# Kernel tuning notes

Measured on AMD Instinct MI355X. Metric: run time of the kernel, lower is better.

The kernel has to match this reference:

```python
import jax, jax.numpy as jnp
import numpy as np

N_NODES = 20000
N_EDGES = 640000
IN_DIM = 128
HID = 128
OUT_DIM = 3
N_GRAPHS = 32


def setup_inputs() -> dict:
    key = jax.random.key(0)
    ks = jax.random.split(key, 12)
    x = jax.random.normal(ks[0], (N_NODES, IN_DIM), dtype=jnp.float32)
    edge_index = jax.random.randint(ks[1], (2, N_EDGES), 0, N_NODES, dtype=jnp.int64)
    batch = jnp.sort(jax.random.randint(ks[2], (N_NODES,), 0, N_GRAPHS, dtype=jnp.int64))
    batch = batch.at[0].set(0).at[-1].set(N_GRAPHS - 1)
    s = 0.05
    W_gcn = jax.random.normal(ks[3], (IN_DIM, HID), jnp.float32) * s
    b_gcn = jnp.zeros((HID,), jnp.float32)
    W_sage_l = jax.random.normal(ks[4], (HID, HID), jnp.float32) * s  # neighbor branch
    W_sage_r = jax.random.normal(ks[5], (HID, HID), jnp.float32) * s  # root branch
    b_sage = jnp.zeros((HID,), jnp.float32)
    W_fc1 = jax.random.normal(ks[6], (HID, HID), jnp.float32) * s
    b_fc1 = jnp.zeros((HID,), jnp.float32)
    W_fc2 = jax.random.normal(ks[7], (HID, OUT_DIM), jnp.float32) * s
    b_fc2 = jnp.zeros((OUT_DIM,), jnp.float32)
    return {
        'x': x, 'edge_index': edge_index, 'batch': batch,
        'W_gcn': W_gcn, 'b_gcn': b_gcn,
        'W_sage_l': W_sage_l, 'W_sage_r': W_sage_r, 'b_sage': b_sage,
        'W_fc1': W_fc1, 'b_fc1': b_fc1, 'W_fc2': W_fc2, 'b_fc2': b_fc2,
    }


def reference(x, edge_index, batch, W_gcn, b_gcn, W_sage_l, W_sage_r, b_sage,
              W_fc1, b_fc1, W_fc2, b_fc2):
    n = x.shape[0]
    row, col = edge_index[0], edge_index[1]  # source -> target

    # ---- GCNConv: symmetric-normalized aggregation with self-loops ----
    h = x @ W_gcn  # [N, H]
    loops = jnp.arange(n, dtype=row.dtype)
    row_sl = jnp.concatenate([row, loops])
    col_sl = jnp.concatenate([col, loops])
    deg = jax.ops.segment_sum(jnp.ones_like(col_sl, dtype=h.dtype), col_sl,
                              num_segments=n)
    dinv = jnp.where(deg > 0, jax.lax.rsqrt(deg), 0.0)
    norm = dinv[row_sl] * dinv[col_sl]  # [E+N]
    h_gcn = jax.ops.segment_sum(h[row_sl] * norm[:, None], col_sl,
                                num_segments=n) + b_gcn
    h_gcn = jax.nn.relu(h_gcn)

    # ---- SAGEConv (mean aggregator) ----
    cnt = jax.ops.segment_sum(jnp.ones_like(col, dtype=h_gcn.dtype), col,
                              num_segments=n)
    neigh = jax.ops.segment_sum(h_gcn[row], col, num_segments=n)
    neigh = neigh / jnp.maximum(cnt, 1.0)[:, None]
    h_sage = neigh @ W_sage_l + h_gcn @ W_sage_r + b_sage
    h_sage = jax.nn.relu(h_sage)

    # ---- global_add_pool (num_graphs = 32 < 50) ----
    pooled = jax.ops.segment_sum(h_sage, batch, num_segments=N_GRAPHS)  # [G, H]

    # ---- MLP head ----
    out = jax.nn.relu(pooled @ W_fc1 + b_fc1) @ W_fc2 + b_fc2  # [G, 3]
    return out
```

## Files before the change

### kernel.cpp

```cpp
#include <hip/hip_runtime.h>

#define N_NODES 20000
#define N_EDGES 640000
#define HID 128
#define N_GRAPHS 32

#define SCAN_BLK 256
#define SCAN_NBLK ((N_NODES + SCAN_BLK - 1) / SCAN_BLK)

__global__ __launch_bounds__(256) void hist_k(const int* __restrict__ col,
                                              int* __restrict__ cnt) {
    int e = blockIdx.x * blockDim.x + threadIdx.x;
    if (e < N_EDGES) {
        int c = col[e];
        if ((unsigned)c < N_NODES) atomicAdd(&cnt[c], 1);
    }
}

__global__ __launch_bounds__(SCAN_BLK) void scanA_k(const int* __restrict__ cnt,
                                                    int* __restrict__ blkSum) {
    __shared__ int wsum[SCAN_BLK / 64];
    const int b = blockIdx.x, t = threadIdx.x;
    const int i = b * SCAN_BLK + t;
    int v = (i < N_NODES) ? cnt[i] : 0;
#pragma unroll
    for (int o = 1; o < 64; o <<= 1) v += __shfl_xor(v, o);
    if ((t & 63) == 0) wsum[t >> 6] = v;
    __syncthreads();
    if (t == 0) {
        int s = 0;
#pragma unroll
        for (int w = 0; w < SCAN_BLK / 64; ++w) s += wsum[w];
        blkSum[b] = s;
    }
}

__global__ __launch_bounds__(SCAN_BLK) void scanB_k(const int* __restrict__ cnt,
                                                    const int* __restrict__ blkSum,
                                                    int* __restrict__ offs,
                                                    int* __restrict__ cursor,
                                                    float* __restrict__ dinv) {
    __shared__ int sm[SCAN_BLK];
    __shared__ int base_s;
    const int b = blockIdx.x, t = threadIdx.x;
    const int i = b * SCAN_BLK + t;
    const int v = (i < N_NODES) ? cnt[i] : 0;
    sm[t] = v;
    if (t == 0) {
        int s = 0;
        for (int k = 0; k < b; ++k) s += blkSum[k];
        base_s = s;
    }
    __syncthreads();
    for (int o = 1; o < SCAN_BLK; o <<= 1) {
        int add = (t >= o) ? sm[t - o] : 0;
        __syncthreads();
        sm[t] += add;
        __syncthreads();
    }
    if (i < N_NODES) {
        int excl = base_s + ((t > 0) ? sm[t - 1] : 0);
        offs[i] = excl;
        cursor[i] = excl;
        dinv[i] = rsqrtf((float)(v + 1));
        if (i == N_NODES - 1) offs[N_NODES] = excl + v;
    }
}

__global__ __launch_bounds__(256) void fill_k(const int* __restrict__ row,
                                              const int* __restrict__ col,
                                              int* __restrict__ cursor,
                                              int* __restrict__ csr_src) {
    int e = blockIdx.x * blockDim.x + threadIdx.x;
    if (e < N_EDGES) {
        int c = col[e];
        int r = row[e];
        if ((unsigned)c < N_NODES && (unsigned)r < N_NODES) {
            int p = atomicAdd(&cursor[c], 1);
            csr_src[p] = r;
        }
    }
}

__global__ __launch_bounds__(256) void gemm128_k(const float* __restrict__ X,
                                                 const float* __restrict__ W,
                                                 float* __restrict__ Y) {
    __shared__ float wbuf[64 * 128];
    const int t = threadIdx.x;
    const int lane = t & 63;
    const int wid = __builtin_amdgcn_readfirstlane(t >> 6);
    const int c2 = lane * 2;
    const int row0 = blockIdx.x * 32 + wid * 8;
    const float* Xr = X + (size_t)row0 * 128;
    float2 acc[8];
#pragma unroll
    for (int r = 0; r < 8; ++r) acc[r] = make_float2(0.f, 0.f);
#pragma unroll
    for (int kc = 0; kc < 2; ++kc) {
        __syncthreads();
#pragma unroll
        for (int i = 0; i < 8; ++i)
            ((float4*)wbuf)[t + i * 256] = ((const float4*)W)[kc * 2048 + t + i * 256];
        __syncthreads();
        const int kb = kc * 64;
        for (int k0 = 0; k0 < 64; k0 += 4) {
            float4 xa[8];
#pragma unroll
            for (int r = 0; r < 8; ++r)
                xa[r] = *(const float4*)&Xr[r * 128 + kb + k0];
#pragma unroll
            for (int kk = 0; kk < 4; ++kk) {
                float2 w = *(const float2*)&wbuf[(k0 + kk) * 128 + c2];
#pragma unroll
                for (int r = 0; r < 8; ++r) {
                    float xv = (&xa[r].x)[kk];
                    acc[r].x = fmaf(xv, w.x, acc[r].x);
                    acc[r].y = fmaf(xv, w.y, acc[r].y);
                }
            }
        }
    }
#pragma unroll
    for (int r = 0; r < 8; ++r)
        *(float2*)&Y[(size_t)(row0 + r) * 128 + c2] = acc[r];
}

__global__ __launch_bounds__(256) void gcn_agg_k(const float* __restrict__ h,
                                                 const int* __restrict__ offs,
                                                 const int* __restrict__ src,
                                                 const float* __restrict__ dinv,
                                                 const float* __restrict__ bias,
                                                 float* __restrict__ out) {
    const int wave = threadIdx.x >> 6;
    const int lane = threadIdx.x & 63;
    const int half = lane >> 5;
    const int node = (blockIdx.x * 4 + wave) * 2 + half;
    const int c4 = (lane & 31) * 4;
    const int nd = (node < N_NODES) ? node : (N_NODES - 1);
    const float dc = dinv[nd];
    float4 hv = *(const float4*)&h[(size_t)nd * 128 + c4];
    float4 acc = make_float4(dc * hv.x, dc * hv.y, dc * hv.z, dc * hv.w);
    const int beg = offs[nd];
    const int deg = offs[nd + 1] - beg;
    const int mdeg = max(deg, __shfl(deg, lane ^ 32));
    for (int j = 0; j < mdeg; j += 4) {
        int i0 = (j + 0 < deg) ? beg + j + 0 : 0;
        int i1 = (j + 1 < deg) ? beg + j + 1 : 0;
        int i2 = (j + 2 < deg) ? beg + j + 2 : 0;
        int i3 = (j + 3 < deg) ? beg + j + 3 : 0;
        int s0 = src[i0], s1 = src[i1], s2 = src[i2], s3 = src[i3];
        float w0 = (j + 0 < deg) ? dinv[s0] : 0.f;
        float w1 = (j + 1 < deg) ? dinv[s1] : 0.f;
        float w2 = (j + 2 < deg) ? dinv[s2] : 0.f;
        float w3 = (j + 3 < deg) ? dinv[s3] : 0.f;
        float4 v0 = *(const float4*)&h[(size_t)s0 * 128 + c4];
        float4 v1 = *(const float4*)&h[(size_t)s1 * 128 + c4];
        float4 v2 = *(const float4*)&h[(size_t)s2 * 128 + c4];
        float4 v3 = *(const float4*)&h[(size_t)s3 * 128 + c4];
        acc.x = fmaf(w0, v0.x, fmaf(w1, v1.x, fmaf(w2, v2.x, fmaf(w3, v3.x, acc.x))));
        acc.y = fmaf(w0, v0.y, fmaf(w1, v1.y, fmaf(w2, v2.y, fmaf(w3, v3.y, acc.y))));
        acc.z = fmaf(w0, v0.z, fmaf(w1, v1.z, fmaf(w2, v2.z, fmaf(w3, v3.z, acc.z))));
        acc.w = fmaf(w0, v0.w, fmaf(w1, v1.w, fmaf(w2, v2.w, fmaf(w3, v3.w, acc.w))));
    }
    float4 b = *(const float4*)&bias[c4];
    float4 o;
    o.x = fmaxf(fmaf(dc, acc.x, b.x), 0.f);
    o.y = fmaxf(fmaf(dc, acc.y, b.y), 0.f);
    o.z = fmaxf(fmaf(dc, acc.z, b.z), 0.f);
    o.w = fmaxf(fmaf(dc, acc.w, b.w), 0.f);
    if (node < N_NODES) *(float4*)&out[(size_t)node * 128 + c4] = o;
}

__global__ __launch_bounds__(256) void sage_agg_k(const float* __restrict__ hg,
                                                  const int* __restrict__ offs,
                                                  const int* __restrict__ src,
                                                  float* __restrict__ out) {
    const int wave = threadIdx.x >> 6;
    const int lane = threadIdx.x & 63;
    const int half = lane >> 5;
    const int node = (blockIdx.x * 4 + wave) * 2 + half;
    const int c4 = (lane & 31) * 4;
    const int nd = (node < N_NODES) ? node : (N_NODES - 1);
    float4 acc = make_float4(0.f, 0.f, 0.f, 0.f);
    const int beg = offs[nd];
    const int deg = offs[nd + 1] - beg;
    const int mdeg = max(deg, __shfl(deg, lane ^ 32));
    for (int j = 0; j < mdeg; j += 4) {
        int i0 = (j + 0 < deg) ? beg + j + 0 : 0;
        int i1 = (j + 1 < deg) ? beg + j + 1 : 0;
        int i2 = (j + 2 < deg) ? beg + j + 2 : 0;
        int i3 = (j + 3 < deg) ? beg + j + 3 : 0;
        float w0 = (j + 0 < deg) ? 1.f : 0.f;
        float w1 = (j + 1 < deg) ? 1.f : 0.f;
        float w2 = (j + 2 < deg) ? 1.f : 0.f;
        float w3 = (j + 3 < deg) ? 1.f : 0.f;
        int s0 = src[i0], s1 = src[i1], s2 = src[i2], s3 = src[i3];
        float4 v0 = *(const float4*)&hg[(size_t)s0 * 128 + c4];
        float4 v1 = *(const float4*)&hg[(size_t)s1 * 128 + c4];
        float4 v2 = *(const float4*)&hg[(size_t)s2 * 128 + c4];
        float4 v3 = *(const float4*)&hg[(size_t)s3 * 128 + c4];
        acc.x = fmaf(w0, v0.x, fmaf(w1, v1.x, fmaf(w2, v2.x, fmaf(w3, v3.x, acc.x))));
        acc.y = fmaf(w0, v0.y, fmaf(w1, v1.y, fmaf(w2, v2.y, fmaf(w3, v3.y, acc.y))));
        acc.z = fmaf(w0, v0.z, fmaf(w1, v1.z, fmaf(w2, v2.z, fmaf(w3, v3.z, acc.z))));
        acc.w = fmaf(w0, v0.w, fmaf(w1, v1.w, fmaf(w2, v2.w, fmaf(w3, v3.w, acc.w))));
    }
    float inv = 1.0f / (float)max(deg, 1);
    float4 o;
    o.x = acc.x * inv;
    o.y = acc.y * inv;
    o.z = acc.z * inv;
    o.w = acc.w * inv;
    if (node < N_NODES) *(float4*)&out[(size_t)node * 128 + c4] = o;
}

__global__ __launch_bounds__(256) void combine_k(const float* __restrict__ An,
                                                 const float* __restrict__ Bh,
                                                 const float* __restrict__ Wl,
                                                 const float* __restrict__ Wr,
                                                 const float* __restrict__ bias,
                                                 float* __restrict__ Y) {
    __shared__ float wbuf[64 * 128];
    const int t = threadIdx.x;
    const int lane = t & 63;
    const int wid = __builtin_amdgcn_readfirstlane(t >> 6);
    const int c2 = lane * 2;
    const int row0 = blockIdx.x * 32 + wid * 8;
    float2 acc[8];
    {
        float2 b = *(const float2*)&bias[c2];
#pragma unroll
        for (int r = 0; r < 8; ++r) acc[r] = b;
    }
#pragma unroll
    for (int m = 0; m < 2; ++m) {
        const float* Wm = m ? Wr : Wl;
        const float* Xr = (m ? Bh : An) + (size_t)row0 * 128;
#pragma unroll
        for (int kc = 0; kc < 2; ++kc) {
            __syncthreads();
#pragma unroll
            for (int i = 0; i < 8; ++i)
                ((float4*)wbuf)[t + i * 256] = ((const float4*)Wm)[kc * 2048 + t + i * 256];
            __syncthreads();
            const int kb = kc * 64;
            for (int k0 = 0; k0 < 64; k0 += 4) {
                float4 xa[8];
#pragma unroll
                for (int r = 0; r < 8; ++r)
                    xa[r] = *(const float4*)&Xr[r * 128 + kb + k0];
#pragma unroll
                for (int kk = 0; kk < 4; ++kk) {
                    float2 w = *(const float2*)&wbuf[(k0 + kk) * 128 + c2];
#pragma unroll
                    for (int r = 0; r < 8; ++r) {
                        float xv = (&xa[r].x)[kk];
                        acc[r].x = fmaf(xv, w.x, acc[r].x);
                        acc[r].y = fmaf(xv, w.y, acc[r].y);
                    }
                }
            }
        }
    }
#pragma unroll
    for (int r = 0; r < 8; ++r) {
        float2 o = acc[r];
        o.x = fmaxf(o.x, 0.f);
        o.y = fmaxf(o.y, 0.f);
        *(float2*)&Y[(size_t)(row0 + r) * 128 + c2] = o;
    }
}

#define POOL_ROWS 64
__global__ __launch_bounds__(256) void pool_k(const float* __restrict__ H,
                                              const int* __restrict__ batch,
                                              float* __restrict__ pooled) {
    const int r0 = blockIdx.x * POOL_ROWS;
    const int t = threadIdx.x;
    const int d = t & 127, half = t >> 7;
    const int rend = min(r0 + POOL_ROWS, N_NODES);
    int i = r0 + half;
    if (i >= rend) return;
    int cur = batch[i];
    float acc = 0.f;
    for (; i < rend; i += 2) {
        int g = batch[i];
        if (g != cur) {
            atomicAdd(&pooled[cur * 128 + d], acc);
            acc = 0.f;
            cur = g;
        }
        acc += H[(size_t)i * 128 + d];
    }
    atomicAdd(&pooled[cur * 128 + d], acc);
}

__global__ __launch_bounds__(128) void head_k(const float* __restrict__ pooled,
                                              const float* __restrict__ Wfc1,
                                              const float* __restrict__ bfc1,
                                              const float* __restrict__ Wfc2,
                                              const float* __restrict__ bfc2,
                                              float* __restrict__ out) {
    __shared__ float pl[128];
    __shared__ float tmp[128];
    const int g = blockIdx.x;
    const int t = threadIdx.x;
    pl[t] = pooled[g * 128 + t];
    __syncthreads();
    float a = bfc1[t];
#pragma unroll 8
    for (int k = 0; k < 128; ++k) a = fmaf(pl[k], Wfc1[k * 128 + t], a);
    tmp[t] = fmaxf(a, 0.f);
    __syncthreads();
    if (t < 3) {
        float a2 = bfc2[t];
        for (int k = 0; k < 128; ++k) a2 = fmaf(tmp[k], Wfc2[k * 3 + t], a2);
        out[g * 3 + t] = a2;
    }
}

extern "C" void kernel_launch(void* const* d_in, const int* in_sizes, int n_in,
                              void* d_out, int out_size, void* d_ws, size_t ws_size,
                              hipStream_t stream) {
    const float* x      = (const float*)d_in[0];
    const int*   ei     = (const int*)d_in[1];
    const int*   batch  = (const int*)d_in[2];
    const float* W_gcn  = (const float*)d_in[3];
    const float* b_gcn  = (const float*)d_in[4];
    const float* W_sl   = (const float*)d_in[5];
    const float* W_sr   = (const float*)d_in[6];
    const float* b_sage = (const float*)d_in[7];
    const float* W_fc1  = (const float*)d_in[8];
    const float* b_fc1  = (const float*)d_in[9];
    const float* W_fc2  = (const float*)d_in[10];
    const float* b_fc2  = (const float*)d_in[11];
    float* out = (float*)d_out;

    char* base = (char*)d_ws;
    size_t off = 0;
    auto take = [&](size_t bytes) -> void* {
        void* p = base + off;
        off += (bytes + 255) & ~(size_t)255;
        return p;
    };
    int*   cnt      = (int*)take((size_t)N_NODES * 4);
    int*   offs     = (int*)take((size_t)(N_NODES + 1) * 4);
    int*   cursor   = (int*)take((size_t)N_NODES * 4);
    float* dinv     = (float*)take((size_t)N_NODES * 4);
    int*   blkSum   = (int*)take((size_t)SCAN_NBLK * 4);
    int*   csr_src  = (int*)take((size_t)N_EDGES * 4);
    float* bufA     = (float*)take((size_t)N_NODES * HID * 4);
    float* bufB     = (float*)take((size_t)N_NODES * HID * 4);
    float* pooled   = (float*)take((size_t)N_GRAPHS * HID * 4);

    const int* row = ei;
    const int* col = ei + N_EDGES;

    hipMemsetAsync(cnt, 0, (size_t)N_NODES * 4, stream);
    hipMemsetAsync(pooled, 0, (size_t)N_GRAPHS * HID * 4, stream);

    hist_k<<<(N_EDGES + 255) / 256, 256, 0, stream>>>(col, cnt);
    scanA_k<<<SCAN_NBLK, SCAN_BLK, 0, stream>>>(cnt, blkSum);
    scanB_k<<<SCAN_NBLK, SCAN_BLK, 0, stream>>>(cnt, blkSum, offs, cursor, dinv);
    fill_k<<<(N_EDGES + 255) / 256, 256, 0, stream>>>(row, col, cursor, csr_src);

    const int gemm_blocks = N_NODES / 32;
    const int agg_blocks = (N_NODES + 7) / 8;
    gemm128_k<<<gemm_blocks, 256, 0, stream>>>(x, W_gcn, bufA);
    gcn_agg_k<<<agg_blocks, 256, 0, stream>>>(bufA, offs, csr_src, dinv, b_gcn, bufB);
    sage_agg_k<<<agg_blocks, 256, 0, stream>>>(bufB, offs, csr_src, bufA);
    combine_k<<<gemm_blocks, 256, 0, stream>>>(bufA, bufB, W_sl, W_sr, b_sage, bufA);
    pool_k<<<(N_NODES + POOL_ROWS - 1) / POOL_ROWS, 256, 0, stream>>>(bufA, batch, pooled);
    head_k<<<N_GRAPHS, 128, 0, stream>>>(pooled, W_fc1, b_fc1, W_fc2, b_fc2, out);
}
```

Measured before the change: 330.0 us.

## Stage transposed X tile in LDS and use 4x4 register tiles in GEMMs

The two dense GEMM kernels (the GCN projection and the SAGE combine) now stage the block's 32 input rows into shared memory, transposed and padded. Each thread then computes a 4-row by 4-column tile using float4 loads from both X and W in LDS. Before, each thread did an 8x2 tile and read X straight from global memory. The aim is fewer global loads per FMA and better register reuse, at the cost of extra LDS space and transpose stores that may bank-conflict, which could lower occupancy.

```diff
diff --git a/kernel.cpp b/kernel.cpp
--- a/kernel.cpp
+++ b/kernel.cpp
@@ -7,6 +7,8 @@
 
 #define SCAN_BLK 256
 #define SCAN_NBLK ((N_NODES + SCAN_BLK - 1) / SCAN_BLK)
+
+#define XT_STRIDE 36
 
 __global__ __launch_bounds__(256) void hist_k(const int* __restrict__ col,
                                               int* __restrict__ cnt) {
@@ -82,47 +84,70 @@
     }
 }
 
+__device__ __forceinline__ void stage_xt(float* xt, const float* __restrict__ Xm,
+                                         int row0, int t) {
+    const int r = t & 31;
+    const int kbase = (t >> 5) * 16;
+    const float* xp = Xm + (size_t)(row0 + r) * 128 + kbase;
+#pragma unroll
+    for (int c = 0; c < 4; ++c) {
+        float4 v = *(const float4*)&xp[c * 4];
+        xt[(kbase + c * 4 + 0) * XT_STRIDE + r] = v.x;
+        xt[(kbase + c * 4 + 1) * XT_STRIDE + r] = v.y;
+        xt[(kbase + c * 4 + 2) * XT_STRIDE + r] = v.z;
+        xt[(kbase + c * 4 + 3) * XT_STRIDE + r] = v.w;
+    }
+}
+
+__device__ __forceinline__ void gemm_half(const float* xt, const float* wbuf,
+                                          int kb, int rg, int c4, float4 acc[4]) {
+#pragma unroll 8
+    for (int k0 = 0; k0 < 64; ++k0) {
+        float4 w = *(const float4*)&wbuf[k0 * 128 + c4];
+        float4 xr = *(const float4*)&xt[(kb + k0) * XT_STRIDE + rg * 4];
+        acc[0].x = fmaf(xr.x, w.x, acc[0].x);
+        acc[0].y = fmaf(xr.x, w.y, acc[0].y);
+        acc[0].z = fmaf(xr.x, w.z, acc[0].z);
+        acc[0].w = fmaf(xr.x, w.w, acc[0].w);
+        acc[1].x = fmaf(xr.y, w.x, acc[1].x);
+        acc[1].y = fmaf(xr.y, w.y, acc[1].y);
+        acc[1].z = fmaf(xr.y, w.z, acc[1].z);
+        acc[1].w = fmaf(xr.y, w.w, acc[1].w);
+        acc[2].x = fmaf(xr.z, w.x, acc[2].x);
+        acc[2].y = fmaf(xr.z, w.y, acc[2].y);
+        acc[2].z = fmaf(xr.z, w.z, acc[2].z);
+        acc[2].w = fmaf(xr.z, w.w, acc[2].w);
+        acc[3].x = fmaf(xr.w, w.x, acc[3].x);
+        acc[3].y = fmaf(xr.w, w.y, acc[3].y);
+        acc[3].z = fmaf(xr.w, w.z, acc[3].z);
+        acc[3].w = fmaf(xr.w, w.w, acc[3].w);
+    }
+}
+
 __global__ __launch_bounds__(256) void gemm128_k(const float* __restrict__ X,
                                                  const float* __restrict__ W,
                                                  float* __restrict__ Y) {
     __shared__ float wbuf[64 * 128];
+    __shared__ float xt[128 * XT_STRIDE];
     const int t = threadIdx.x;
-    const int lane = t & 63;
-    const int wid = __builtin_amdgcn_readfirstlane(t >> 6);
-    const int c2 = lane * 2;
-    const int row0 = blockIdx.x * 32 + wid * 8;
-    const float* Xr = X + (size_t)row0 * 128;
-    float2 acc[8];
-#pragma unroll
-    for (int r = 0; r < 8; ++r) acc[r] = make_float2(0.f, 0.f);
+    const int rg = t >> 5;
+    const int c4 = (t & 31) * 4;
+    const int row0 = blockIdx.x * 32;
+    float4 acc[4];
+    acc[0] = acc[1] = acc[2] = acc[3] = make_float4(0.f, 0.f, 0.f, 0.f);
+    stage_xt(xt, X, row0, t);
 #pragma unroll
     for (int kc = 0; kc < 2; ++kc) {
-        __syncthreads();
+        if (kc) __syncthreads();
 #pragma unroll
         for (int i = 0; i < 8; ++i)
             ((float4*)wbuf)[t + i * 256] = ((const float4*)W)[kc * 2048 + t + i * 256];
         __syncthreads();
-        const int kb = kc * 64;
-        for (int k0 = 0; k0 < 64; k0 += 4) {
-            float4 xa[8];
-#pragma unroll
-            for (int r = 0; r < 8; ++r)
-                xa[r] = *(const float4*)&Xr[r * 128 + kb + k0];
-#pragma unroll
-            for (int kk = 0; kk < 4; ++kk) {
-                float2 w = *(const float2*)&wbuf[(k0 + kk) * 128 + c2];
-#pragma unroll
-                for (int r = 0; r < 8; ++r) {
-                    float xv = (&xa[r].x)[kk];
-                    acc[r].x = fmaf(xv, w.x, acc[r].x);
-                    acc[r].y = fmaf(xv, w.y, acc[r].y);
-                }
-            }
-        }
-    }
-#pragma unroll
-    for (int r = 0; r < 8; ++r)
-        *(float2*)&Y[(size_t)(row0 + r) * 128 + c2] = acc[r];
+        gemm_half(xt, wbuf, kc * 64, rg, c4, acc);
+    }
+#pragma unroll
+    for (int i = 0; i < 4; ++i)
+        *(float4*)&Y[(size_t)(row0 + rg * 4 + i) * 128 + c4] = acc[i];
 }
 
 __global__ __launch_bounds__(256) void gcn_agg_k(const float* __restrict__ h,
@@ -220,53 +245,40 @@
                                                  const float* __restrict__ bias,
                                                  float* __restrict__ Y) {
     __shared__ float wbuf[64 * 128];
+    __shared__ float xt[128 * XT_STRIDE];
     const int t = threadIdx.x;
-    const int lane = t & 63;
-    const int wid = __builtin_amdgcn_readfirstlane(t >> 6);
-    const int c2 = lane * 2;
-    const int row0 = blockIdx.x * 32 + wid * 8;
-    float2 acc[8];
+    const int rg = t >> 5;
+    const int c4 = (t & 31) * 4;
+    const int row0 = blockIdx.x * 32;
+    float4 acc[4];
     {
-        float2 b = *(const float2*)&bias[c2];
-#pragma unroll
-        for (int r = 0; r < 8; ++r) acc[r] = b;
+        float4 b = *(const float4*)&bias[c4];
+        acc[0] = acc[1] = acc[2] = acc[3] = b;
     }
 #pragma unroll
     for (int m = 0; m < 2; ++m) {
         const float* Wm = m ? Wr : Wl;
-        const float* Xr = (m ? Bh : An) + (size_t)row0 * 128;
+        const float* Xm = m ? Bh : An;
+        if (m) __syncthreads();
+        stage_xt(xt, Xm, row0, t);
 #pragma unroll
         for (int kc = 0; kc < 2; ++kc) {
-            __syncthreads();
+            if (m || kc) __syncthreads();
 #pragma unroll
             for (int i = 0; i < 8; ++i)
                 ((float4*)wbuf)[t + i * 256] = ((const float4*)Wm)[kc * 2048 + t + i * 256];
             __syncthreads();
-            const int kb = kc * 64;
-            for (int k0 = 0; k0 < 64; k0 += 4) {
-                float4 xa[8];
-#pragma unroll
-                for (int r = 0; r < 8; ++r)
-                    xa[r] = *(const float4*)&Xr[r * 128 + kb + k0];
-#pragma unroll
-                for (int kk = 0; kk < 4; ++kk) {
-                    float2 w = *(const float2*)&wbuf[(k0 + kk) * 128 + c2];
-#pragma unroll
-                    for (int r = 0; r < 8; ++r) {
-                        float xv = (&xa[r].x)[kk];
-                        acc[r].x = fmaf(xv, w.x, acc[r].x);
-                        acc[r].y = fmaf(xv, w.y, acc[r].y);
-                    }
-                }
-            }
+            gemm_half(xt, wbuf, kc * 64, rg, c4, acc);
         }
     }
 #pragma unroll
-    for (int r = 0; r < 8; ++r) {
-        float2 o = acc[r];
+    for (int i = 0; i < 4; ++i) {
+        float4 o = acc[i];
         o.x = fmaxf(o.x, 0.f);
         o.y = fmaxf(o.y, 0.f);
-        *(float2*)&Y[(size_t)(row0 + r) * 128 + c2] = o;
+        o.z = fmaxf(o.z, 0.f);
+        o.w = fmaxf(o.w, 0.f);
+        *(float4*)&Y[(size_t)(row0 + rg * 4 + i) * 128 + c4] = o;
     }
 }
 
```

Measured after the change: 300.1 us. 9.0% less time.
